# Optimization experiments

Hardware: AMD Instinct MI355X
Metric: run time of the kernel (lower is better)

The kernel has to match this reference:

```python
import jax, jax.numpy as jnp
import numpy as np

N = 50000
E = 1600000
IN = 128
HID = 32
HEADS = 4
SLOPE = 0.2   # GATConv default negative_slope
EPS = 1e-5    # BatchNorm eps


def setup_inputs() -> dict:
    key = jax.random.key(0)
    ks = jax.random.split(key, 16)
    inp = {}
    inp["x"] = jax.random.normal(ks[0], (N, IN), dtype=jnp.float32)
    inp["edge_index"] = jax.random.randint(ks[1], (2, E), 0, N, dtype=jnp.int32)
    def p(k, shape, s=0.1):
        return jax.random.normal(k, shape, dtype=jnp.float32) * s
    # layer dims: (in_ch, out_ch_per_head, heads, concat)
    dims = [(IN, HID, HEADS, True), (HID * HEADS, HID, HEADS, True), (HID * HEADS, HID, 1, False)]
    i = 2
    for li, (ic, oc, h, concat) in enumerate(dims):
        inp[f"W{li}"] = p(ks[i], (ic, h * oc)); i += 1
        inp[f"as{li}"] = p(ks[i], (h, oc)); i += 1
        inp[f"ad{li}"] = p(ks[i], (h, oc)); i += 1
        bn_dim = h * oc if concat else oc
        inp[f"b{li}"] = jnp.zeros((bn_dim,), jnp.float32)
        inp[f"g{li}"] = jnp.ones((bn_dim,), jnp.float32)
        inp[f"be{li}"] = jnp.zeros((bn_dim,), jnp.float32)
    inp["cw1"] = p(ks[i], (HID, HID // 2)); i += 1
    inp["cb1"] = jnp.zeros((HID // 2,), jnp.float32)
    inp["cw2"] = p(ks[i], (HID // 2, 2)); i += 1
    inp["cb2"] = jnp.zeros((2,), jnp.float32)
    return inp


def _gat_layer(h, src, dst, W, a_s, a_d, b, heads, oc, concat):
    # PyG GATConv: x -> [N,H,C]; alpha = softmax_dst(leaky_relu(a_s.x_src + a_d.x_dst))
    n = h.shape[0]
    x = (h @ W).reshape(n, heads, oc)                 # [N,H,C]
    e_s = (x * a_s).sum(-1)                            # [N,H]
    e_d = (x * a_d).sum(-1)                            # [N,H]
    e = jax.nn.leaky_relu(e_s[src] + e_d[dst], SLOPE)  # [Etot,H]
    m = jax.ops.segment_max(e, dst, num_segments=n)    # segment softmax over dst
    ex = jnp.exp(e - m[dst])
    den = jax.ops.segment_sum(ex, dst, num_segments=n)
    alpha = ex / (den[dst] + 1e-16)                    # [Etot,H]
    out = jax.ops.segment_sum(x[src] * alpha[:, :, None], dst, num_segments=n)  # [N,H,C]
    out = out.reshape(n, heads * oc) if concat else out.mean(1)
    return out + b


def _bn(x, g, be):
    mu = x.mean(0)
    var = x.var(0)  # biased, as torch BN uses for normalization
    return g * (x - mu) * jax.lax.rsqrt(var + EPS) + be


def reference(x, edge_index, W0, as0, ad0, b0, g0, be0, W1, as1, ad1, b1, g1, be1,
              W2, as2, ad2, b2, g2, be2, cw1, cb1, cw2, cb2):
    n = x.shape[0]
    loops = jnp.arange(n, dtype=edge_index.dtype)      # add_self_loops=True default
    src = jnp.concatenate([edge_index[0], loops])
    dst = jnp.concatenate([edge_index[1], loops])
    layers = [(W0, as0, ad0, b0, g0, be0, HEADS, HID, True),
              (W1, as1, ad1, b1, g1, be1, HEADS, HID, True),
              (W2, as2, ad2, b2, g2, be2, 1, HID, False)]
    h = x
    for (W, a_s, a_d, b, g, be, heads, oc, concat) in layers:
        h = _gat_layer(h, src, dst, W, a_s, a_d, b, heads, oc, concat)
        h = jax.nn.elu(_bn(h, g, be))
    h = jax.nn.elu(h @ cw1 + cb1)
    return h @ cw2 + cb2
```

## Files before the change

kernel.cpp:

```cpp
#include <hip/hip_runtime.h>

static constexpr float SLOPE = 0.2f;
static constexpr float BN_EPS = 1e-5f;

static inline int cdiv(long long a, long long b) { return (int)((a + b - 1) / b); }

typedef __attribute__((ext_vector_type(8))) short short8;
typedef __attribute__((ext_vector_type(4))) float f32x4;

__device__ __forceinline__ unsigned short f2bf(float f) {
  unsigned u = __float_as_uint(f);
  u += 0x7fff + ((u >> 16) & 1);
  return (unsigned short)(u >> 16);
}
__device__ __forceinline__ float bf2f(unsigned short h) {
  return __uint_as_float((unsigned)h << 16);
}

static constexpr int EPB = 8192;
static constexpr int BCAP = 12288;

__global__ void prep_hist(const int* __restrict__ ei, int* __restrict__ counts,
                          const float* __restrict__ W0, const float* __restrict__ W1,
                          const float* __restrict__ W2,
                          unsigned short* __restrict__ Wt0, unsigned short* __restrict__ Wt1,
                          unsigned short* __restrict__ Wt2,
                          float* __restrict__ sums0, float* __restrict__ sums1,
                          float* __restrict__ sums2,
                          int E, int NBLK, int NB) {
  const int tid = threadIdx.x;
  const int blk = blockIdx.x;
  if (blk < NBLK) {
    __shared__ int cnt[256];
    cnt[tid] = 0;
    __syncthreads();
    const int i0 = blk * EPB;
    const int i1 = min(E, i0 + EPB);
    for (int i = i0 + tid; i < i1; i += 256) atomicAdd(&cnt[ei[E + i] >> 8], 1);
    __syncthreads();
    if (tid < NB) counts[tid * NBLK + blk] = cnt[tid];
    return;
  }
  const int b = blk - NBLK;
  if (b < 64) {
    int o = b * 256 + tid;
    int j = o >> 7, k = o & 127;
    Wt0[o] = f2bf(W0[k * 128 + j]);
  } else if (b < 128) {
    int o = (b - 64) * 256 + tid;
    int j = o >> 7, k = o & 127;
    Wt1[o] = f2bf(W1[k * 128 + j]);
  } else if (b < 144) {
    int o = (b - 128) * 256 + tid;
    int j = o >> 7, k = o & 127;
    Wt2[o] = f2bf(W2[k * 32 + j]);
  } else {
    sums0[tid] = 0.f;
    sums1[tid] = 0.f;
    if (tid < 64) sums2[tid] = 0.f;
  }
}

__global__ void csr_scan2(const int* __restrict__ counts, int* __restrict__ offsets, int m) {
  __shared__ int wtot[16];
  const int tid = threadIdx.x;
  const int lane = tid & 63, wv = tid >> 6;
  const int CH = (m + 1023) >> 10;
  const int lo = min(m, tid * CH);
  const int hi = min(m, lo + CH);
  int sum = 0;
  for (int i = lo; i < hi; ++i) sum += counts[i];
  int x = sum;
#pragma unroll
  for (int off = 1; off < 64; off <<= 1) {
    int y = __shfl_up(x, off);
    if (lane >= off) x += y;
  }
  if (lane == 63) wtot[wv] = x;
  __syncthreads();
  int add = 0;
  for (int w = 0; w < wv; ++w) add += wtot[w];
  int run = x - sum + add;
  for (int i = lo; i < hi; ++i) { offsets[i] = run; run += counts[i]; }
  if (hi == m) offsets[m] = run;
}

__global__ __launch_bounds__(256) void csr_part(const int* __restrict__ ei,
                                                const int* __restrict__ offsets,
                                                unsigned* __restrict__ ebuf,
                                                int E, int NBLK, int NB) {
  __shared__ unsigned stage[EPB];
  __shared__ int cnt[256], sstart[256], cur[256], goff[256];
  __shared__ int wtot[4];
  const int tid = threadIdx.x;
  const int blk = blockIdx.x;
  const int lane = tid & 63, wv = tid >> 6;
  cnt[tid] = 0;
  if (tid < NB) goff[tid] = offsets[tid * NBLK + blk];
  __syncthreads();
  const int i0 = blk * EPB;
  const int i1 = min(E, i0 + EPB);
  for (int i = i0 + tid; i < i1; i += 256) atomicAdd(&cnt[ei[E + i] >> 8], 1);
  __syncthreads();
  int v = cnt[tid];
  int x = v;
#pragma unroll
  for (int off = 1; off < 64; off <<= 1) {
    int y = __shfl_up(x, off);
    if (lane >= off) x += y;
  }
  if (lane == 63) wtot[wv] = x;
  __syncthreads();
  int add = 0;
  for (int w = 0; w < wv; ++w) add += wtot[w];
  int excl = x - v + add;
  sstart[tid] = excl;
  cur[tid] = excl;
  __syncthreads();
  for (int i = i0 + tid; i < i1; i += 256) {
    int s = ei[i], d = ei[E + i];
    int p = atomicAdd(&cur[d >> 8], 1);
    stage[p] = ((unsigned)s << 8) | (unsigned)(d & 255);
  }
  __syncthreads();
  for (int b = wv; b < NB; b += 4) {
    const int ls = sstart[b], le = cur[b];
    const int gbase = goff[b];
    for (int e = ls + lane; e < le; e += 64) ebuf[gbase + (e - ls)] = stage[e];
  }
}

__global__ __launch_bounds__(256) void csr_bucket(const unsigned* __restrict__ ebuf,
                                                  const int* __restrict__ offsets,
                                                  int* __restrict__ row_start,
                                                  int* __restrict__ csr_src,
                                                  int n, int E, int NBLK, int NB) {
  __shared__ unsigned stage[BCAP];
  __shared__ int deg[256], cur[256];
  __shared__ int wtot[4];
  const int b = blockIdx.x;
  const int base = b << 8;
  const int nn = min(256, n - base);
  const int estart = offsets[b * NBLK];
  const int eend = (b + 1 < NB) ? offsets[(b + 1) * NBLK] : E;
  const int gstart = estart + base;
  const int tid = threadIdx.x;
  const int lane = tid & 63, wv = tid >> 6;
  deg[tid] = (tid < nn) ? 1 : 0;
  __syncthreads();
  for (int j = estart + tid; j < eend; j += 256) atomicAdd(&deg[ebuf[j] & 255u], 1);
  __syncthreads();
  int v = deg[tid];
  int x = v;
#pragma unroll
  for (int off = 1; off < 64; off <<= 1) {
    int y = __shfl_up(x, off);
    if (lane >= off) x += y;
  }
  if (lane == 63) wtot[wv] = x;
  __syncthreads();
  int add = 0;
  for (int w = 0; w < wv; ++w) add += wtot[w];
  int excl = x - v + add;
  cur[tid] = excl;
  if (tid < nn) row_start[base + tid] = gstart + excl;
  if (b == 0 && tid == 0) row_start[n] = E + n;
  __syncthreads();
  if (tid < nn) {
    int p = atomicAdd(&cur[tid], 1);
    if (p < BCAP) stage[p] = (unsigned)(base + tid);
    else csr_src[gstart + p] = base + tid;
  }
  for (int j = estart + tid; j < eend; j += 256) {
    unsigned pk = ebuf[j];
    int p = atomicAdd(&cur[pk & 255u], 1);
    if (p < BCAP) stage[p] = pk >> 8;
    else csr_src[gstart + p] = (int)(pk >> 8);
  }
  __syncthreads();
  const int tot = min(eend - estart + nn, BCAP);
  for (int e = tid; e < tot; e += 256) csr_src[gstart + e] = (int)stage[e];
}

template<int IC, int OC, int H, bool BN, bool AF32>
__global__ void gemm_mfma(const unsigned short* __restrict__ Act,
                          const float* __restrict__ Axf,
                          const unsigned short* __restrict__ Wt,
                          const float* __restrict__ a_s, const float* __restrict__ a_d,
                          const float* __restrict__ bnsums, const float* __restrict__ g,
                          const float* __restrict__ be,
                          unsigned short* __restrict__ Pb, float* __restrict__ es,
                          float* __restrict__ ed, int n) {
  constexpr int NF = OC / 16;
  __shared__ float s_sc[IC], s_sf[IC];
  __shared__ unsigned short s_stage[4 * 16 * OC];
  const int tid = threadIdx.x;
  if (BN) {
    const float inv_n = 1.f / (float)n;
    for (int c = tid; c < IC; c += 256) {
      float mu = bnsums[c] * inv_n;
      float var = bnsums[IC + c] * inv_n - mu * mu;
      float s = g[c] * rsqrtf(var + BN_EPS);
      s_sc[c] = s;
      s_sf[c] = be[c] - mu * s;
    }
    __syncthreads();
  }
  const int lane = tid & 63;
  const int l15 = lane & 15;
  const int lk = lane >> 4;
  const int wid = tid >> 6;
  const int node0 = blockIdx.x * 64 + wid * 16;
  const int arow = node0 + l15;
  const int ar = AF32 ? min(arow, n - 1) : arow;

  f32x4 acc[NF];
#pragma unroll
  for (int cb = 0; cb < NF; ++cb) acc[cb] = (f32x4){0.f, 0.f, 0.f, 0.f};

#pragma unroll
  for (int kc = 0; kc < IC / 32; ++kc) {
    const int kbase = kc * 32 + lk * 8;
    short8 a;
    if (AF32) {
      float4 u0 = *(const float4*)(Axf + (size_t)ar * IC + kbase);
      float4 u1 = *(const float4*)(Axf + (size_t)ar * IC + kbase + 4);
      a[0] = (short)f2bf(u0.x); a[1] = (short)f2bf(u0.y);
      a[2] = (short)f2bf(u0.z); a[3] = (short)f2bf(u0.w);
      a[4] = (short)f2bf(u1.x); a[5] = (short)f2bf(u1.y);
      a[6] = (short)f2bf(u1.z); a[7] = (short)f2bf(u1.w);
    } else {
      a = *(const short8*)(Act + (size_t)ar * IC + kbase);
    }
    if (BN) {
      short8 ta;
#pragma unroll
      for (int i = 0; i < 8; ++i) {
        float v = bf2f((unsigned short)a[i]);
        float y = fmaf(v, s_sc[kbase + i], s_sf[kbase + i]);
        y = (y > 0.f) ? y : (__expf(y) - 1.f);
        ta[i] = (short)f2bf(y);
      }
      a = ta;
    }
#pragma unroll
    for (int cb = 0; cb < NF; ++cb) {
      short8 b = *(const short8*)(Wt + (size_t)(cb * 16 + l15) * IC + kbase);
      acc[cb] = __builtin_amdgcn_mfma_f32_16x16x32_bf16(a, b, acc[cb], 0, 0, 0);
    }
  }

  unsigned short* st = s_stage + wid * 16 * OC;
  float esum[4] = {0.f, 0.f, 0.f, 0.f}, edum[4] = {0.f, 0.f, 0.f, 0.f};
#pragma unroll
  for (int cb = 0; cb < NF; ++cb) {
    const int j = cb * 16 + l15;
    const float asv = a_s[j];
    const float adv = a_d[j];
#pragma unroll
    for (int i = 0; i < 4; ++i) {
      float p = acc[cb][i];
      st[(lk * 4 + i) * OC + j] = f2bf(p);
      float ps = p * asv, pd = p * adv;
#pragma unroll
      for (int mm = 1; mm <= 8; mm <<= 1) {
        ps += __shfl_xor(ps, mm);
        pd += __shfl_xor(pd, mm);
      }
      esum[i] += ps;
      edum[i] += pd;
    }
    if (cb & 1) {
      const int h = cb >> 1;
#pragma unroll
      for (int i = 0; i < 4; ++i) {
        int node = node0 + lk * 4 + i;
        if (l15 == 0 && node < n) {
          es[node * H + h] = esum[i];
          ed[node * H + h] = edum[i];
        }
        esum[i] = 0.f;
        edum[i] = 0.f;
      }
    }
  }
  for (int idx = lane; idx < 2 * OC; idx += 64) {
    int r = idx / (OC / 8);
    int q = idx % (OC / 8);
    int node = node0 + r;
    if (node < n)
      *(uint4*)(Pb + (size_t)node * OC + q * 8) = *(const uint4*)(st + r * OC + q * 8);
  }
}

template<int H, int C>
__global__ void node_agg(const int* __restrict__ row_start, const int* __restrict__ csr_src,
                         const float* __restrict__ es, const float* __restrict__ ed,
                         const unsigned short* __restrict__ Pb, unsigned short* __restrict__ Ob,
                         int n) {
  constexpr int HC = H * C;
  constexpr int TPN = HC / 8;
  const int tid = threadIdx.x;
  const int t = tid % TPN;
  const int node = blockIdx.x * (256 / TPN) + tid / TPN;
  if (node >= n) return;
  const int h = (t * 8) / C;
  const int e0 = row_start[node];
  const int e1 = row_start[node + 1];
  const float edd = ed[node * H + h];
  const uint4* P4 = (const uint4*)Pb;
  float a0 = 0.f, a1 = 0.f, a2 = 0.f, a3 = 0.f;
  float a4 = 0.f, a5 = 0.f, a6 = 0.f, a7 = 0.f;
  float den = 0.f;
  int s0 = csr_src[e0];
  int s1 = (e0 + 1 < e1) ? csr_src[e0 + 1] : s0;
  int s2 = (e0 + 2 < e1) ? csr_src[e0 + 2] : s0;
  int s3 = (e0 + 3 < e1) ? csr_src[e0 + 3] : s0;
  for (int j = e0; j < e1; j += 4) {
    const int nj = j + 4;
    int t0 = (nj     < e1) ? csr_src[nj]     : s0;
    int t1 = (nj + 1 < e1) ? csr_src[nj + 1] : s0;
    int t2 = (nj + 2 < e1) ? csr_src[nj + 2] : s0;
    int t3 = (nj + 3 < e1) ? csr_src[nj + 3] : s0;
    float x0 = es[s0 * H + h], x1 = es[s1 * H + h];
    float x2 = es[s2 * H + h], x3 = es[s3 * H + h];
    uint4 p0 = P4[(size_t)s0 * TPN + t];
    uint4 p1 = P4[(size_t)s1 * TPN + t];
    uint4 p2 = P4[(size_t)s2 * TPN + t];
    uint4 p3 = P4[(size_t)s3 * TPN + t];
    x0 += edd; x0 = fmaxf(x0, SLOPE * x0);
    x1 += edd; x1 = fmaxf(x1, SLOPE * x1);
    x2 += edd; x2 = fmaxf(x2, SLOPE * x2);
    x3 += edd; x3 = fmaxf(x3, SLOPE * x3);
    float w0 = __expf(x0);
    float w1 = (j + 1 < e1) ? __expf(x1) : 0.f;
    float w2 = (j + 2 < e1) ? __expf(x2) : 0.f;
    float w3 = (j + 3 < e1) ? __expf(x3) : 0.f;
    den += (w0 + w1) + (w2 + w3);
    a0 = fmaf(w0, __uint_as_float(p0.x << 16), a0);
    a1 = fmaf(w0, __uint_as_float(p0.x & 0xffff0000u), a1);
    a2 = fmaf(w0, __uint_as_float(p0.y << 16), a2);
    a3 = fmaf(w0, __uint_as_float(p0.y & 0xffff0000u), a3);
    a4 = fmaf(w0, __uint_as_float(p0.z << 16), a4);
    a5 = fmaf(w0, __uint_as_float(p0.z & 0xffff0000u), a5);
    a6 = fmaf(w0, __uint_as_float(p0.w << 16), a6);
    a7 = fmaf(w0, __uint_as_float(p0.w & 0xffff0000u), a7);
    a0 = fmaf(w1, __uint_as_float(p1.x << 16), a0);
    a1 = fmaf(w1, __uint_as_float(p1.x & 0xffff0000u), a1);
    a2 = fmaf(w1, __uint_as_float(p1.y << 16), a2);
    a3 = fmaf(w1, __uint_as_float(p1.y & 0xffff0000u), a3);
    a4 = fmaf(w1, __uint_as_float(p1.z << 16), a4);
    a5 = fmaf(w1, __uint_as_float(p1.z & 0xffff0000u), a5);
    a6 = fmaf(w1, __uint_as_float(p1.w << 16), a6);
    a7 = fmaf(w1, __uint_as_float(p1.w & 0xffff0000u), a7);
    a0 = fmaf(w2, __uint_as_float(p2.x << 16), a0);
    a1 = fmaf(w2, __uint_as_float(p2.x & 0xffff0000u), a1);
    a2 = fmaf(w2, __uint_as_float(p2.y << 16), a2);
    a3 = fmaf(w2, __uint_as_float(p2.y & 0xffff0000u), a3);
    a4 = fmaf(w2, __uint_as_float(p2.z << 16), a4);
    a5 = fmaf(w2, __uint_as_float(p2.z & 0xffff0000u), a5);
    a6 = fmaf(w2, __uint_as_float(p2.w << 16), a6);
    a7 = fmaf(w2, __uint_as_float(p2.w & 0xffff0000u), a7);
    a0 = fmaf(w3, __uint_as_float(p3.x << 16), a0);
    a1 = fmaf(w3, __uint_as_float(p3.x & 0xffff0000u), a1);
    a2 = fmaf(w3, __uint_as_float(p3.y << 16), a2);
    a3 = fmaf(w3, __uint_as_float(p3.y & 0xffff0000u), a3);
    a4 = fmaf(w3, __uint_as_float(p3.z << 16), a4);
    a5 = fmaf(w3, __uint_as_float(p3.z & 0xffff0000u), a5);
    a6 = fmaf(w3, __uint_as_float(p3.w << 16), a6);
    a7 = fmaf(w3, __uint_as_float(p3.w & 0xffff0000u), a7);
    s0 = t0; s1 = t1; s2 = t2; s3 = t3;
  }
  float inv = 1.f / (den + 1e-16f);
  uint4 o;
  o.x = (unsigned)f2bf(a0 * inv) | ((unsigned)f2bf(a1 * inv) << 16);
  o.y = (unsigned)f2bf(a2 * inv) | ((unsigned)f2bf(a3 * inv) << 16);
  o.z = (unsigned)f2bf(a4 * inv) | ((unsigned)f2bf(a5 * inv) << 16);
  o.w = (unsigned)f2bf(a6 * inv) | ((unsigned)f2bf(a7 * inv) << 16);
  *(uint4*)(Ob + (size_t)node * HC + t * 8) = o;
}

template<int C>
__global__ __launch_bounds__(1024) void bn_stats3(const unsigned short* __restrict__ X,
                                                  float* __restrict__ sums, int n) {
  constexpr int TPR = C / 4;
  constexpr int RPB = 1024 / TPR;
  __shared__ float ls[2 * C];
  const int tid = threadIdx.x;
  if (tid < 2 * C) ls[tid] = 0.f;
  __syncthreads();
  const int c4 = (tid % TPR) * 4;
  const int rb = tid / TPR;
  float s0 = 0.f, s1 = 0.f, s2 = 0.f, s3 = 0.f;
  float q0 = 0.f, q1 = 0.f, q2 = 0.f, q3 = 0.f;
  for (int r = blockIdx.x * RPB + rb; r < n; r += gridDim.x * RPB) {
    uint2 v = *(const uint2*)(X + (size_t)r * C + c4);
    float f0 = __uint_as_float(v.x << 16);
    float f1 = __uint_as_float(v.x & 0xffff0000u);
    float f2 = __uint_as_float(v.y << 16);
    float f3 = __uint_as_float(v.y & 0xffff0000u);
    s0 += f0; q0 = fmaf(f0, f0, q0);
    s1 += f1; q1 = fmaf(f1, f1, q1);
    s2 += f2; q2 = fmaf(f2, f2, q2);
    s3 += f3; q3 = fmaf(f3, f3, q3);
  }
  atomicAdd(&ls[c4 + 0], s0);
  atomicAdd(&ls[c4 + 1], s1);
  atomicAdd(&ls[c4 + 2], s2);
  atomicAdd(&ls[c4 + 3], s3);
  atomicAdd(&ls[C + c4 + 0], q0);
  atomicAdd(&ls[C + c4 + 1], q1);
  atomicAdd(&ls[C + c4 + 2], q2);
  atomicAdd(&ls[C + c4 + 3], q3);
  __syncthreads();
  if (tid < 2 * C) unsafeAtomicAdd(&sums[tid], ls[tid]);
}

__global__ void mlp_head(const unsigned short* __restrict__ Hf, const float* __restrict__ bnsums,
                         const float* __restrict__ g, const float* __restrict__ be,
                         const float* __restrict__ cw1, const float* __restrict__ cb1,
                         const float* __restrict__ cw2, const float* __restrict__ cb2,
                         float* __restrict__ out, int n) {
  __shared__ float w1[32 * 16];
  __shared__ float b1[16];
  __shared__ float w2[16 * 2];
  __shared__ float b2[2];
  __shared__ float sc[32], sf[32];
  int tid = threadIdx.x;
  for (int i = tid; i < 32 * 16; i += blockDim.x) w1[i] = cw1[i];
  if (tid < 16) b1[tid] = cb1[tid];
  if (tid < 32) w2[tid] = cw2[tid];
  if (tid < 2) b2[tid] = cb2[tid];
  if (tid < 32) {
    float inv_n = 1.f / (float)n;
    float mu = bnsums[tid] * inv_n;
    float var = bnsums[32 + tid] * inv_n - mu * mu;
    float s = g[tid] * rsqrtf(var + BN_EPS);
    sc[tid] = s;
    sf[tid] = be[tid] - mu * s;
  }
  __syncthreads();
  int node = blockIdx.x * blockDim.x + tid;
  if (node >= n) return;
  float x[32];
  const uint4* xp = (const uint4*)(Hf + (size_t)node * 32);
#pragma unroll
  for (int q = 0; q < 4; ++q) {
    uint4 v = xp[q];
    unsigned pr[4] = {v.x, v.y, v.z, v.w};
#pragma unroll
    for (int u = 0; u < 4; ++u) {
      int c = q * 8 + u * 2;
      float va = __uint_as_float(pr[u] << 16);
      float vb = __uint_as_float(pr[u] & 0xffff0000u);
      float ya = fmaf(va, sc[c], sf[c]);
      float yb = fmaf(vb, sc[c + 1], sf[c + 1]);
      x[c] = (ya > 0.f) ? ya : (__expf(ya) - 1.f);
      x[c + 1] = (yb > 0.f) ? yb : (__expf(yb) - 1.f);
    }
  }
  float o0 = b2[0], o1 = b2[1];
#pragma unroll
  for (int j = 0; j < 16; ++j) {
    float acc = b1[j];
#pragma unroll
    for (int k = 0; k < 32; ++k) acc = fmaf(x[k], w1[k * 16 + j], acc);
    acc = (acc > 0.f) ? acc : (__expf(acc) - 1.f);
    o0 = fmaf(acc, w2[j * 2 + 0], o0);
    o1 = fmaf(acc, w2[j * 2 + 1], o1);
  }
  out[(size_t)node * 2 + 0] = o0;
  out[(size_t)node * 2 + 1] = o1;
}

extern "C" void kernel_launch(void* const* d_in, const int* in_sizes, int n_in,
                              void* d_out, int out_size, void* d_ws, size_t ws_size,
                              hipStream_t stream) {
  const float* x   = (const float*)d_in[0];
  const int*   ei  = (const int*)d_in[1];
  const float* W0  = (const float*)d_in[2];
  const float* as0 = (const float*)d_in[3];
  const float* ad0 = (const float*)d_in[4];
  const float* g0  = (const float*)d_in[6];
  const float* be0 = (const float*)d_in[7];
  const float* W1  = (const float*)d_in[8];
  const float* as1 = (const float*)d_in[9];
  const float* ad1 = (const float*)d_in[10];
  const float* g1  = (const float*)d_in[12];
  const float* be1 = (const float*)d_in[13];
  const float* W2  = (const float*)d_in[14];
  const float* as2 = (const float*)d_in[15];
  const float* ad2 = (const float*)d_in[16];
  const float* g2  = (const float*)d_in[18];
  const float* be2 = (const float*)d_in[19];
  const float* cw1 = (const float*)d_in[20];
  const float* cb1 = (const float*)d_in[21];
  const float* cw2 = (const float*)d_in[22];
  const float* cb2 = (const float*)d_in[23];

  const int n = in_sizes[0] / 128;
  const int E = in_sizes[1] / 2;
  const int n64 = cdiv(n, 64) * 64;

  const int NBLK = cdiv(E, EPB);
  const int NB = cdiv(n, 256);
  const int m = NB * NBLK;

  unsigned short* Ab  = (unsigned short*)d_ws;
  unsigned short* Bb  = Ab + (size_t)n64 * 128;
  unsigned short* Pb  = Bb + (size_t)n64 * 128;
  unsigned short* Af  = Pb + (size_t)n64 * 128;
  unsigned short* Wt0 = Af + (size_t)n64 * 32;
  unsigned short* Wt1 = Wt0 + 128 * 128;
  unsigned short* Wt2 = Wt1 + 128 * 128;
  float* es    = (float*)(Wt2 + 32 * 128);
  float* ed    = es + (size_t)n * 4;
  float* sums0 = ed + (size_t)n * 4;
  float* sums1 = sums0 + 256;
  float* sums2 = sums1 + 256;
  int* counts    = (int*)(sums2 + 64);
  int* offsets   = counts + m;
  int* row_start = offsets + m + 1;
  int* csr_src   = row_start + n + 1;
  unsigned* ebuf = (unsigned*)(csr_src + E + n);

  prep_hist<<<NBLK + 145, 256, 0, stream>>>(ei, counts, W0, W1, W2, Wt0, Wt1, Wt2,
                                            sums0, sums1, sums2, E, NBLK, NB);
  csr_scan2<<<1, 1024, 0, stream>>>(counts, offsets, m);
  csr_part<<<NBLK, 256, 0, stream>>>(ei, offsets, ebuf, E, NBLK, NB);
  csr_bucket<<<NB, 256, 0, stream>>>(ebuf, offsets, row_start, csr_src, n, E, NBLK, NB);

  gemm_mfma<128, 128, 4, false, true><<<cdiv(n, 64), 256, 0, stream>>>(
      nullptr, x, Wt0, as0, ad0, nullptr, nullptr, nullptr, Pb, es, ed, n);
  node_agg<4, 32><<<cdiv(n, 16), 256, 0, stream>>>(row_start, csr_src, es, ed, Pb, Ab, n);
  bn_stats3<128><<<64, 1024, 0, stream>>>(Ab, sums0, n);

  gemm_mfma<128, 128, 4, true, false><<<cdiv(n, 64), 256, 0, stream>>>(
      Ab, nullptr, Wt1, as1, ad1, sums0, g0, be0, Pb, es, ed, n);
  node_agg<4, 32><<<cdiv(n, 16), 256, 0, stream>>>(row_start, csr_src, es, ed, Pb, Bb, n);
  bn_stats3<128><<<64, 1024, 0, stream>>>(Bb, sums1, n);

  gemm_mfma<128, 32, 1, true, false><<<cdiv(n, 64), 256, 0, stream>>>(
      Bb, nullptr, Wt2, as2, ad2, sums1, g1, be1, Pb, es, ed, n);
  node_agg<1, 32><<<cdiv(n, 64), 256, 0, stream>>>(row_start, csr_src, es, ed, Pb, Af, n);
  bn_stats3<32><<<64, 1024, 0, stream>>>(Af, sums2, n);

  mlp_head<<<cdiv(n, 256), 256, 0, stream>>>(Af, sums2, g2, be2, cw1, cb1, cw2, cb2,
                                             (float*)d_out, n);
}
```

Measured before the change: 394.0 us.

## Sort nodes by degree to balance per-wave work in aggregation kernels

Builds a degree histogram while bucketing the CSR, scans it, and produces a node permutation ordered by in-degree. The three aggregation kernels then walk nodes through this permutation, so lanes in a wave handle nodes of similar degree and do not idle waiting on high-degree neighbours. In exchange it adds two small kernels and an extra indirection, and the output writes now land in scattered order rather than in contiguous node order.

Measured after the change: 600.8 us. +52.5%, slower.

```diff
diff --git a/kernel.cpp b/kernel.cpp
--- a/kernel.cpp
+++ b/kernel.cpp
@@ -26,7 +26,7 @@
                           unsigned short* __restrict__ Wt0, unsigned short* __restrict__ Wt1,
                           unsigned short* __restrict__ Wt2,
                           float* __restrict__ sums0, float* __restrict__ sums1,
-                          float* __restrict__ sums2,
+                          float* __restrict__ sums2, int* __restrict__ dhist,
                           int E, int NBLK, int NB) {
   const int tid = threadIdx.x;
   const int blk = blockIdx.x;
@@ -58,6 +58,7 @@
     sums0[tid] = 0.f;
     sums1[tid] = 0.f;
     if (tid < 64) sums2[tid] = 0.f;
+    dhist[tid] = 0;
   }
 }
 
@@ -134,6 +135,7 @@
                                                   const int* __restrict__ offsets,
                                                   int* __restrict__ row_start,
                                                   int* __restrict__ csr_src,
+                                                  int* __restrict__ dhist,
                                                   int n, int E, int NBLK, int NB) {
   __shared__ unsigned stage[BCAP];
   __shared__ int deg[256], cur[256];
@@ -150,6 +152,7 @@
   __syncthreads();
   for (int j = estart + tid; j < eend; j += 256) atomicAdd(&deg[ebuf[j] & 255u], 1);
   __syncthreads();
+  if (tid < nn) atomicAdd(&dhist[min(deg[tid], 255)], 1);
   int v = deg[tid];
   int x = v;
 #pragma unroll
@@ -180,6 +183,32 @@
   __syncthreads();
   const int tot = min(eend - estart + nn, BCAP);
   for (int e = tid; e < tot; e += 256) csr_src[gstart + e] = (int)stage[e];
+}
+
+__global__ void dscan(const int* __restrict__ dhist, int* __restrict__ dcur) {
+  const int lane = threadIdx.x;
+  int v[4];
+  int s = 0;
+#pragma unroll
+  for (int i = 0; i < 4; ++i) { v[i] = dhist[lane * 4 + i]; s += v[i]; }
+  int x = s;
+#pragma unroll
+  for (int off = 1; off < 64; off <<= 1) {
+    int y = __shfl_up(x, off);
+    if (lane >= off) x += y;
+  }
+  int run = x - s;
+#pragma unroll
+  for (int i = 0; i < 4; ++i) { dcur[lane * 4 + i] = run; run += v[i]; }
+}
+
+__global__ void dperm(const int* __restrict__ row_start, int* __restrict__ dcur,
+                      int* __restrict__ nperm, int n) {
+  int node = blockIdx.x * blockDim.x + threadIdx.x;
+  if (node >= n) return;
+  int d = min(row_start[node + 1] - row_start[node], 255);
+  int pos = atomicAdd(&dcur[d], 1);
+  nperm[pos] = node;
 }
 
 template<int IC, int OC, int H, bool BN, bool AF32>
@@ -294,7 +323,8 @@
 }
 
 template<int H, int C>
-__global__ void node_agg(const int* __restrict__ row_start, const int* __restrict__ csr_src,
+__global__ void node_agg(const int* __restrict__ nperm, const int* __restrict__ row_start,
+                         const int* __restrict__ csr_src,
                          const float* __restrict__ es, const float* __restrict__ ed,
                          const unsigned short* __restrict__ Pb, unsigned short* __restrict__ Ob,
                          int n) {
@@ -302,8 +332,9 @@
   constexpr int TPN = HC / 8;
   const int tid = threadIdx.x;
   const int t = tid % TPN;
-  const int node = blockIdx.x * (256 / TPN) + tid / TPN;
-  if (node >= n) return;
+  const int idx = blockIdx.x * (256 / TPN) + tid / TPN;
+  if (idx >= n) return;
+  const int node = nperm[idx];
   const int h = (t * 8) / C;
   const int e0 = row_start[node];
   const int e1 = row_start[node + 1];
@@ -518,31 +549,36 @@
   float* sums0 = ed + (size_t)n * 4;
   float* sums1 = sums0 + 256;
   float* sums2 = sums1 + 256;
-  int* counts    = (int*)(sums2 + 64);
+  int* dhist     = (int*)(sums2 + 64);
+  int* dcur      = dhist + 256;
+  int* nperm     = dcur + 256;
+  int* counts    = nperm + n;
   int* offsets   = counts + m;
   int* row_start = offsets + m + 1;
   int* csr_src   = row_start + n + 1;
   unsigned* ebuf = (unsigned*)(csr_src + E + n);
 
   prep_hist<<<NBLK + 145, 256, 0, stream>>>(ei, counts, W0, W1, W2, Wt0, Wt1, Wt2,
-                                            sums0, sums1, sums2, E, NBLK, NB);
+                                            sums0, sums1, sums2, dhist, E, NBLK, NB);
   csr_scan2<<<1, 1024, 0, stream>>>(counts, offsets, m);
   csr_part<<<NBLK, 256, 0, stream>>>(ei, offsets, ebuf, E, NBLK, NB);
-  csr_bucket<<<NB, 256, 0, stream>>>(ebuf, offsets, row_start, csr_src, n, E, NBLK, NB);
+  csr_bucket<<<NB, 256, 0, stream>>>(ebuf, offsets, row_start, csr_src, dhist, n, E, NBLK, NB);
+  dscan<<<1, 64, 0, stream>>>(dhist, dcur);
+  dperm<<<cdiv(n, 256), 256, 0, stream>>>(row_start, dcur, nperm, n);
 
   gemm_mfma<128, 128, 4, false, true><<<cdiv(n, 64), 256, 0, stream>>>(
       nullptr, x, Wt0, as0, ad0, nullptr, nullptr, nullptr, Pb, es, ed, n);
-  node_agg<4, 32><<<cdiv(n, 16), 256, 0, stream>>>(row_start, csr_src, es, ed, Pb, Ab, n);
+  node_agg<4, 32><<<cdiv(n, 16), 256, 0, stream>>>(nperm, row_start, csr_src, es, ed, Pb, Ab, n);
   bn_stats3<128><<<64, 1024, 0, stream>>>(Ab, sums0, n);
 
   gemm_mfma<128, 128, 4, true, false><<<cdiv(n, 64), 256, 0, stream>>>(
       Ab, nullptr, Wt1, as1, ad1, sums0, g0, be0, Pb, es, ed, n);
-  node_agg<4, 32><<<cdiv(n, 16), 256, 0, stream>>>(row_start, csr_src, es, ed, Pb, Bb, n);
+  node_agg<4, 32><<<cdiv(n, 16), 256, 0, stream>>>(nperm, row_start, csr_src, es, ed, Pb, Bb, n);
   bn_stats3<128><<<64, 1024, 0, stream>>>(Bb, sums1, n);
 
   gemm_mfma<128, 32, 1, true, false><<<cdiv(n, 64), 256, 0, stream>>>(
       Bb, nullptr, Wt2, as2, ad2, sums1, g1, be1, Pb, es, ed, n);
-  node_agg<1, 32><<<cdiv(n, 64), 256, 0, stream>>>(row_start, csr_src, es, ed, Pb, Af, n);
+  node_agg<1, 32><<<cdiv(n, 64), 256, 0, stream>>>(nperm, row_start, csr_src, es, ed, Pb, Af, n);
   bn_stats3<32><<<64, 1024, 0, stream>>>(Af, sums2, n);
 
   mlp_head<<<cdiv(n, 256), 256, 0, stream>>>(Af, sums2, g2, be2, cw1, cb1, cw2, cb2,
```
